# Optimization experiments

Hardware: AMD Instinct MI355X
Metric: run time of the kernel (lower is better)

## Reference

```python
import jax, jax.numpy as jnp
import numpy as np

RES = 3.5
K = (np.pi / RES) ** 2          # Gaussian falloff constant
BW2 = 6.0                        # squared neighborhood radius (voxels)
R = 3                            # floor(idx - sqrt(6)) = idx-3, ceil(idx + sqrt(6)) = idx+3


def _offsets():
    o = jnp.arange(-R, R + 1)
    oz, oy, ox = jnp.meshgrid(o, o, o, indexing='ij')
    offs = jnp.stack([oz.ravel(), oy.ravel(), ox.ravel()], axis=-1)  # (343, 3)
    d2 = jnp.sum(offs * offs, axis=-1)                               # (343,)
    return offs, d2


def _splat(coords, x0, y0, z0, vox, G):
    """coords: (N,3) atom positions. Returns (G,G,G) density grid via scatter-max."""
    idx = jnp.stack([
        jnp.floor((coords[:, 0] - x0[0]) / vox[0]),
        jnp.floor((coords[:, 1] - y0[0]) / vox[0]),
        jnp.floor((coords[:, 2] - z0[0]) / vox[0]),
    ], axis=1).astype(jnp.int32)                                     # (N, 3)

    offs, d2 = _offsets()
    pos = idx[:, None, :] + offs[None, :, :]                         # (N, 343, 3)

    M = G - 1                                                        # min(dims) - 1 (cubic grid)
    lc = jnp.clip(idx - R, 0, M)                                     # clamped bbox lower (N,3)
    uc = jnp.clip(idx + R, 0, M)                                     # clamped bbox upper (N,3)
    in_range = jnp.all((pos >= lc[:, None, :]) & (pos <= uc[:, None, :]), axis=-1)
    center_ok = jnp.all((idx >= 0) & (idx < G), axis=-1)             # atom's own voxel inside grid
    valid = in_range & (d2 <= BW2)[None, :] & center_ok[:, None]     # (N, 343)

    prob = jnp.where(valid, jnp.exp(-K * d2.astype(jnp.float32))[None, :], 0.0)

    pos_c = jnp.clip(pos, 0, G - 1)                                  # safe indices for invalid slots
    flat = (pos_c[..., 0] * G + pos_c[..., 1]) * G + pos_c[..., 2]   # (N, 343)

    grid = jnp.zeros((G * G * G,), dtype=jnp.float32)
    grid = grid.at[flat.reshape(-1)].max(prob.reshape(-1))           # scatter-max (grid init 0, prob >= 0)
    return grid.reshape(G, G, G)


def setup_inputs() -> dict:
    key = jax.random.key(0)
    k1, k2 = jax.random.split(key)
    G = 256
    N = 20000
    src = jax.random.uniform(k1, (1, 3, N), dtype=jnp.float32, minval=0.0, maxval=float(G))
    tgt = jax.random.uniform(k2, (1, 3, N), dtype=jnp.float32, minval=0.0, maxval=float(G))
    return {
        'src': src,
        'tgt': tgt,
        'x_origin': jnp.zeros((1,), jnp.float32),
        'y_origin': jnp.zeros((1,), jnp.float32),
        'z_origin': jnp.zeros((1,), jnp.float32),
        'x_voxel': jnp.ones((1,), jnp.float32),
        'grid_dim': G,
    }


def reference(src, tgt, x_origin, y_origin, z_origin, x_voxel, grid_dim):
    G = int(grid_dim)
    src_c = src[0].T                                                 # (N, 3)
    tgt_c = tgt[0].T
    src_mask = _splat(src_c, x_origin, y_origin, z_origin, x_voxel, G)
    tgt_mask = _splat(tgt_c, x_origin, y_origin, z_origin, x_voxel, G)
    # global_alignment_loss: tgt <- tgt*src ; src <- src*src ; loss = mean(sum(src) - sum(tgt))
    rho_em = jnp.sum(tgt_mask * src_mask)
    rho_mo = jnp.sum(src_mask * src_mask)
    return rho_mo - rho_em
```

## Files before the change

kernel.cpp:

```cpp
#include <hip/hip_runtime.h>

#define GDIM   256
#define NCOLS  1024
#define CAP    128
#define NQ     2048

__constant__ int2 OFF01[21] = {
    {-2,-1},{-2,0},{-2,1},
    {-1,-2},{-1,-1},{-1,0},{-1,1},{-1,2},
    { 0,-2},{ 0,-1},{ 0,0},{ 0,1},{ 0,2},
    { 1,-2},{ 1,-1},{ 1,0},{ 1,1},{ 1,2},
    { 2,-1},{ 2,0},{ 2,1},
};
__constant__ unsigned long long PAT01[21] = {
    0x0040204000ull, 0x0020102000ull, 0x0040204000ull,
    0x0040204000ull, 0x4008040840ull, 0x2004020420ull, 0x4008040840ull, 0x0040204000ull,
    0x0020102000ull, 0x2004020420ull, 0x1002010210ull, 0x2004020420ull, 0x0020102000ull,
    0x0040204000ull, 0x4008040840ull, 0x2004020420ull, 0x4008040840ull, 0x0040204000ull,
    0x0040204000ull, 0x0020102000ull, 0x0040204000ull,
};

__global__ void bin_kernel(const float* __restrict__ src,
                           const float* __restrict__ tgt,
                           const float* __restrict__ ox,
                           const float* __restrict__ oy,
                           const float* __restrict__ oz,
                           const float* __restrict__ vox,
                           unsigned* __restrict__ cnt,
                           unsigned* __restrict__ entries,
                           float* __restrict__ out,
                           int N)
{
    int tid = blockIdx.x * blockDim.x + threadIdx.x;
    if (tid == 0) *out = 0.0f;
    if (tid >= 2 * N) return;
    int a = tid % N;
    int m = tid / N;

    const float* c = m ? tgt : src;
    float vx = vox[0];
    int i0 = (int)floorf((c[a]         - ox[0]) / vx);
    int i1 = (int)floorf((c[N + a]     - oy[0]) / vx);
    int i2 = (int)floorf((c[2 * N + a] - oz[0]) / vx);
    if ((unsigned)i0 >= GDIM || (unsigned)i1 >= GDIM || (unsigned)i2 >= GDIM) return;

    unsigned pk = (unsigned)i0 | ((unsigned)i1 << 8) | ((unsigned)i2 << 16);
    int tlx = max(i0 - 2, 0) >> 4, thx = min(i0 + 2, GDIM - 1) >> 4;
    int tly = max(i1 - 2, 0) >> 4, thy = min(i1 + 2, GDIM - 1) >> 4;
    int tlz = max(i2 - 2, 0) >> 6, thz = min(i2 + 2, GDIM - 1) >> 6;

    for (int tx = tlx; tx <= thx; ++tx)
        for (int ty = tly; ty <= thy; ++ty)
            for (int tz = tlz; tz <= thz; ++tz) {
                int bin = m * NCOLS + (((tx << 4) + ty) << 2) + tz;
                unsigned slot = atomicAdd(&cnt[bin], 1u);
                if (slot < CAP) entries[bin * CAP + slot] = pk;
            }
}

__global__ __launch_bounds__(256)
void tile_kernel(const unsigned* __restrict__ cnt,
                 const unsigned* __restrict__ entries,
                 float* __restrict__ out)
{
    __shared__ unsigned long long smem[2 * NQ];
    __shared__ unsigned eS[CAP], eT[CAP];
    __shared__ float tbl[8];
    __shared__ float wsum[4];

    int tid = threadIdx.x;
    int t   = blockIdx.x;
    int cx0 = (t >> 6) << 4;
    int cy0 = ((t >> 2) & 15) << 4;
    int cz0 = (t & 3) << 6;

    if (tid < 8) {
        const float kf = (float)((3.14159265358979323846 / 3.5) * (3.14159265358979323846 / 3.5));
        tbl[tid] = (tid < 7) ? expf(-kf * (float)tid) : 0.0f;
    }
    {
        uint4* zp = (uint4*)smem;
        for (int i = tid; i < 2048; i += 256) zp[i] = make_uint4(0u, 0u, 0u, 0u);
    }
    int nS = min(cnt[t],         (unsigned)CAP);
    int nT = min(cnt[NCOLS + t], (unsigned)CAP);
    for (int i = tid; i < nS; i += 256) eS[i] = entries[t * CAP + i];
    for (int i = tid; i < nT; i += 256) eT[i] = entries[(NCOLS + t) * CAP + i];
    __syncthreads();

    int totS = nS * 21;
    int tot  = totS + nT * 21;
    for (int task = tid; task < tot; task += 256) {
        int m  = task >= totS;
        int lt = m ? task - totS : task;
        int e  = lt / 21, r = lt % 21;
        unsigned pk = m ? eT[e] : eS[e];
        int i0 = pk & 255, i1 = (pk >> 8) & 255, i2 = (pk >> 16) & 255;
        int2 o = OFF01[r];
        int l0 = i0 + o.x - cx0; if ((unsigned)l0 >= 16) continue;
        int l1 = i1 + o.y - cy0; if ((unsigned)l1 >= 16) continue;
        int zs = max(i2 - 2, cz0), ze = min(i2 + 2, cz0 + 63);
        int drop = zs - (i2 - 2), keep = ze - zs + 1;
        unsigned long long pat =
            (PAT01[r] >> (8 * drop)) & ((1ull << (8 * keep)) - 1ull);
        if (!pat) continue;
        int lb  = (l0 << 10) | (l1 << 6) | (zs - cz0);
        int off = lb & 7;
        unsigned long long* q = &smem[m * NQ + (lb >> 3)];
        unsigned long long lo = pat << (8 * off);
        if (lo) atomicOr(q, lo);
        if (off + keep > 8) {
            unsigned long long hi = pat >> (8 * (8 - off));
            if (hi) atomicOr(q + 1, hi);
        }
    }
    __syncthreads();

    float acc = 0.0f;
    const ulonglong2* sp = (const ulonglong2*)smem;
    const ulonglong2* tp = (const ulonglong2*)(smem + NQ);
    for (int i = tid; i < NQ / 2; i += 256) {
        ulonglong2 s = sp[i];
        if ((s.x | s.y) == 0ull) continue;
        ulonglong2 tv = tp[i];
        unsigned long long sv[2] = {s.x, s.y};
        unsigned long long tw[2] = {tv.x, tv.y};
        #pragma unroll
        for (int k = 0; k < 2; ++k) {
            unsigned long long sw  = sv[k];
            unsigned long long twv = tw[k];
            while (sw) {
                int bit  = __ffsll((long long)sw) - 1;
                int byte = bit >> 3;
                float vs = tbl[bit & 7];
                unsigned tb = (unsigned)((twv >> (byte << 3)) & 0xffull);
                float vt = tbl[__ffs((int)(tb | 0x80u)) - 1];
                acc += vs * (vs - vt);
                sw &= ~(0xffull << (byte << 3));
            }
        }
    }
    #pragma unroll
    for (int off2 = 32; off2 > 0; off2 >>= 1)
        acc += __shfl_down(acc, off2, 64);
    int lane = tid & 63, wv = tid >> 6;
    if (lane == 0) wsum[wv] = acc;
    __syncthreads();
    if (tid == 0)
        atomicAdd(out, wsum[0] + wsum[1] + wsum[2] + wsum[3]);
}

extern "C" void kernel_launch(void* const* d_in, const int* in_sizes, int n_in,
                              void* d_out, int out_size, void* d_ws, size_t ws_size,
                              hipStream_t stream)
{
    const float* src = (const float*)d_in[0];
    const float* tgt = (const float*)d_in[1];
    const float* ox  = (const float*)d_in[2];
    const float* oy  = (const float*)d_in[3];
    const float* oz  = (const float*)d_in[4];
    const float* vox = (const float*)d_in[5];
    int N = in_sizes[0] / 3;

    unsigned* cnt     = (unsigned*)d_ws;
    unsigned* entries = cnt + 2 * NCOLS;

    hipMemsetAsync(cnt, 0, 2 * NCOLS * sizeof(unsigned), stream);

    int nb = (2 * N + 255) / 256;
    bin_kernel<<<nb, 256, 0, stream>>>(src, tgt, ox, oy, oz, vox, cnt, entries,
                                       (float*)d_out, N);
    tile_kernel<<<NCOLS, 256, 0, stream>>>(cnt, entries, (float*)d_out);
}
```

Baseline: 97.14 us.

## Restructure tile kernel with per-atom unrolled splats and SWAR byte reductions

Each thread now handles one atom and unrolls all 21 xy-offsets with compile-time offset and pattern tables, replacing the strided task loop with its divide and modulo. The reduction phase no longer walks set bits one at a time. It uses SWAR lowest-set-bit extraction and popcounts to count source-only squared terms per distance, and loops only over bytes where both masks are set, reading a precomputed 49-entry product table. Launch bounds request higher occupancy. The risk is imbalance, since per-thread work now scales with each atom's 21 atomics. The code also assumes at most 256 combined entries, which holds because CAP is 128.

Result: no change. 95.87 us (-1.3%).

```diff
diff --git a/kernel.cpp b/kernel.cpp
--- a/kernel.cpp
+++ b/kernel.cpp
@@ -4,21 +4,6 @@
 #define NCOLS  1024
 #define CAP    128
 #define NQ     2048
-
-__constant__ int2 OFF01[21] = {
-    {-2,-1},{-2,0},{-2,1},
-    {-1,-2},{-1,-1},{-1,0},{-1,1},{-1,2},
-    { 0,-2},{ 0,-1},{ 0,0},{ 0,1},{ 0,2},
-    { 1,-2},{ 1,-1},{ 1,0},{ 1,1},{ 1,2},
-    { 2,-1},{ 2,0},{ 2,1},
-};
-__constant__ unsigned long long PAT01[21] = {
-    0x0040204000ull, 0x0020102000ull, 0x0040204000ull,
-    0x0040204000ull, 0x4008040840ull, 0x2004020420ull, 0x4008040840ull, 0x0040204000ull,
-    0x0020102000ull, 0x2004020420ull, 0x1002010210ull, 0x2004020420ull, 0x0020102000ull,
-    0x0040204000ull, 0x4008040840ull, 0x2004020420ull, 0x4008040840ull, 0x0040204000ull,
-    0x0040204000ull, 0x0020102000ull, 0x0040204000ull,
-};
 
 __global__ void bin_kernel(const float* __restrict__ src,
                            const float* __restrict__ tgt,
@@ -58,15 +43,25 @@
             }
 }
 
-__global__ __launch_bounds__(256)
+__global__ __launch_bounds__(256, 4)
 void tile_kernel(const unsigned* __restrict__ cnt,
                  const unsigned* __restrict__ entries,
                  float* __restrict__ out)
 {
     __shared__ unsigned long long smem[2 * NQ];
     __shared__ unsigned eS[CAP], eT[CAP];
-    __shared__ float tbl[8];
+    __shared__ float tblp[49];
     __shared__ float wsum[4];
+
+    constexpr int OX[21] = {-2,-2,-2,-1,-1,-1,-1,-1, 0, 0, 0, 0, 0, 1, 1, 1, 1, 1, 2, 2, 2};
+    constexpr int OY[21] = {-1, 0, 1,-2,-1, 0, 1, 2,-2,-1, 0, 1, 2,-2,-1, 0, 1, 2,-1, 0, 1};
+    constexpr unsigned long long PATC[21] = {
+        0x0040204000ull, 0x0020102000ull, 0x0040204000ull,
+        0x0040204000ull, 0x4008040840ull, 0x2004020420ull, 0x4008040840ull, 0x0040204000ull,
+        0x0020102000ull, 0x2004020420ull, 0x1002010210ull, 0x2004020420ull, 0x0020102000ull,
+        0x0040204000ull, 0x4008040840ull, 0x2004020420ull, 0x4008040840ull, 0x0040204000ull,
+        0x0040204000ull, 0x0020102000ull, 0x0040204000ull,
+    };
 
     int tid = threadIdx.x;
     int t   = blockIdx.x;
@@ -74,72 +69,95 @@
     int cy0 = ((t >> 2) & 15) << 4;
     int cz0 = (t & 3) << 6;
 
-    if (tid < 8) {
-        const float kf = (float)((3.14159265358979323846 / 3.5) * (3.14159265358979323846 / 3.5));
-        tbl[tid] = (tid < 7) ? expf(-kf * (float)tid) : 0.0f;
+    const float kf = (float)((3.14159265358979323846 / 3.5) * (3.14159265358979323846 / 3.5));
+    if (tid < 49) {
+        int a = tid / 7, b = tid - 7 * a;
+        tblp[tid] = expf(-kf * (float)a) * expf(-kf * (float)b);
     }
     {
         uint4* zp = (uint4*)smem;
-        for (int i = tid; i < 2048; i += 256) zp[i] = make_uint4(0u, 0u, 0u, 0u);
+        #pragma unroll
+        for (int i = 0; i < 8; ++i) zp[tid + i * 256] = make_uint4(0u, 0u, 0u, 0u);
     }
     int nS = min(cnt[t],         (unsigned)CAP);
     int nT = min(cnt[NCOLS + t], (unsigned)CAP);
-    for (int i = tid; i < nS; i += 256) eS[i] = entries[t * CAP + i];
-    for (int i = tid; i < nT; i += 256) eT[i] = entries[(NCOLS + t) * CAP + i];
+    if (tid < nS) eS[tid] = entries[t * CAP + tid];
+    if (tid < nT) eT[tid] = entries[(NCOLS + t) * CAP + tid];
     __syncthreads();
 
-    int totS = nS * 21;
-    int tot  = totS + nT * 21;
-    for (int task = tid; task < tot; task += 256) {
-        int m  = task >= totS;
-        int lt = m ? task - totS : task;
-        int e  = lt / 21, r = lt % 21;
-        unsigned pk = m ? eT[e] : eS[e];
+    if (tid < nS + nT) {
+        int m        = tid >= nS;
+        unsigned pk  = m ? eT[tid - nS] : eS[tid];
         int i0 = pk & 255, i1 = (pk >> 8) & 255, i2 = (pk >> 16) & 255;
-        int2 o = OFF01[r];
-        int l0 = i0 + o.x - cx0; if ((unsigned)l0 >= 16) continue;
-        int l1 = i1 + o.y - cy0; if ((unsigned)l1 >= 16) continue;
-        int zs = max(i2 - 2, cz0), ze = min(i2 + 2, cz0 + 63);
+        int zs   = max(i2 - 2, cz0), ze = min(i2 + 2, cz0 + 63);
         int drop = zs - (i2 - 2), keep = ze - zs + 1;
-        unsigned long long pat =
-            (PAT01[r] >> (8 * drop)) & ((1ull << (8 * keep)) - 1ull);
-        if (!pat) continue;
-        int lb  = (l0 << 10) | (l1 << 6) | (zs - cz0);
-        int off = lb & 7;
-        unsigned long long* q = &smem[m * NQ + (lb >> 3)];
-        unsigned long long lo = pat << (8 * off);
-        if (lo) atomicOr(q, lo);
-        if (off + keep > 8) {
-            unsigned long long hi = pat >> (8 * (8 - off));
-            if (hi) atomicOr(q + 1, hi);
+        int zb   = zs - cz0;
+        int off  = zb & 7;
+        unsigned long long kmask = (1ull << (8 * keep)) - 1ull;
+        int x0 = i0 - cx0, y0 = i1 - cy0;
+        unsigned long long* base = smem + m * NQ;
+        bool spill = (off + keep) > 8;
+        #pragma unroll
+        for (int r = 0; r < 21; ++r) {
+            int l0 = x0 + OX[r]; if ((unsigned)l0 >= 16u) continue;
+            int l1 = y0 + OY[r]; if ((unsigned)l1 >= 16u) continue;
+            unsigned long long pat = (PATC[r] >> (8 * drop)) & kmask;
+            if (!pat) continue;
+            unsigned long long* q = base + (((l0 << 10) | (l1 << 6) | zb) >> 3);
+            unsigned long long lo = pat << (8 * off);
+            if (lo) atomicOr(q, lo);
+            if (spill) {
+                unsigned long long hi = pat >> (8 * (8 - off));
+                if (hi) atomicOr(q + 1, hi);
+            }
         }
     }
     __syncthreads();
 
-    float acc = 0.0f;
+    const unsigned long long H  = 0x8080808080808080ull;
+    const unsigned long long B1 = 0x0101010101010101ull;
+    const unsigned long long K7 = 0x7f7f7f7f7f7f7f7full;
     const ulonglong2* sp = (const ulonglong2*)smem;
     const ulonglong2* tp = (const ulonglong2*)(smem + NQ);
-    for (int i = tid; i < NQ / 2; i += 256) {
-        ulonglong2 s = sp[i];
-        if ((s.x | s.y) == 0ull) continue;
-        ulonglong2 tv = tp[i];
-        unsigned long long sv[2] = {s.x, s.y};
-        unsigned long long tw[2] = {tv.x, tv.y};
+
+    ulonglong2 sv[4], tw[4];
+    #pragma unroll
+    for (int i = 0; i < 4; ++i) {
+        sv[i] = sp[tid + i * 256];
+        tw[i] = tp[tid + i * 256];
+    }
+
+    int cd[7] = {0, 0, 0, 0, 0, 0, 0};
+    float accC = 0.0f;
+    #pragma unroll
+    for (int i = 0; i < 4; ++i) {
         #pragma unroll
         for (int k = 0; k < 2; ++k) {
-            unsigned long long sw  = sv[k];
-            unsigned long long twv = tw[k];
-            while (sw) {
-                int bit  = __ffsll((long long)sw) - 1;
-                int byte = bit >> 3;
-                float vs = tbl[bit & 7];
-                unsigned tb = (unsigned)((twv >> (byte << 3)) & 0xffull);
-                float vt = tbl[__ffs((int)(tb | 0x80u)) - 1];
-                acc += vs * (vs - vt);
-                sw &= ~(0xffull << (byte << 3));
+            unsigned long long w = k ? sv[i].y : sv[i].x;
+            unsigned long long v = k ? tw[i].y : tw[i].x;
+            unsigned long long q   = w | H;
+            unsigned long long lsb = q & (~q + B1);
+            #pragma unroll
+            for (int d = 0; d < 7; ++d)
+                cd[d] += __popcll(lsb & (B1 << d));
+            unsigned long long bth = ((w + K7) & H) & ((v + K7) & H);
+            while (bth) {
+                int bit = __ffsll((long long)bth) - 1;
+                int sh  = bit & ~7;
+                int ds  = __ffs((int)((unsigned)(w >> sh) & 0x7fu)) - 1;
+                int dt  = __ffs((int)((unsigned)(v >> sh) & 0x7fu)) - 1;
+                accC += tblp[ds * 7 + dt];
+                bth &= bth - 1;
             }
         }
     }
+    float acc = -accC;
+    #pragma unroll
+    for (int d = 0; d < 7; ++d) {
+        float tv = expf(-kf * (float)d);
+        acc = fmaf((float)cd[d], tv * tv, acc);
+    }
+
     #pragma unroll
     for (int off2 = 32; off2 > 0; off2 >>= 1)
         acc += __shfl_down(acc, off2, 64);
```
